# Kernel optimization log

Measured on AMD Instinct MI355X. Metric: run time of the kernel, lower is better.

Reference implementation:

```python
import jax, jax.numpy as jnp
import numpy as np

NUM_GRAPHS = 1024
IN_NODE = 128
OUT_GRAPH = 128
N_NODES = 500000

def _xavier(key, shape):
    fan_in, fan_out = shape[1], shape[0]
    a = float(np.sqrt(6.0 / (fan_in + fan_out)))
    return jax.random.uniform(key, shape, jnp.float32, -a, a)

def setup_inputs() -> dict:
    key = jax.random.key(0)
    k = jax.random.split(key, 5)
    x = jax.random.normal(k[0], (N_NODES, IN_NODE), jnp.float32)
    batch = jnp.sort(jax.random.randint(k[1], (N_NODES,), 0, NUM_GRAPHS))
    bias = jnp.full((OUT_GRAPH,), 0.01, jnp.float32)
    return {
        "x": x,
        "batch": batch,
        "W_lin": _xavier(k[2], (OUT_GRAPH, IN_NODE)),
        "b_lin": bias,
        "W_gate": _xavier(k[3], (OUT_GRAPH, IN_NODE)),
        "b_gate": bias,
        "W_final": _xavier(k[4], (OUT_GRAPH, OUT_GRAPH)),
        "b_final": bias,
    }

def reference(x, batch, W_lin, b_lin, W_gate, b_gate, W_final, b_final):
    # node projections: [N, out_graph]
    states = x @ W_lin.T + b_lin
    gates = jax.nn.softmax(x @ W_gate.T + b_gate, axis=1)  # softmax over feature dim
    gated = states * gates
    # scatter_mean over graph ids -> [num_graphs, out_graph]
    sums = jax.ops.segment_sum(gated, batch, num_segments=NUM_GRAPHS)
    counts = jax.ops.segment_sum(jnp.ones((gated.shape[0],), gated.dtype), batch, num_segments=NUM_GRAPHS)
    mean = sums / jnp.clip(counts, 1.0)[:, None]
    return mean @ W_final.T + b_final
```

## Files before the change

### kernel.cpp

```cpp
#include <hip/hip_runtime.h>

typedef __attribute__((ext_vector_type(8))) __bf16 bf16x8;
typedef __attribute__((ext_vector_type(4))) float f32x4;

__device__ __forceinline__ bf16x8 cvt8(f32x4 a, f32x4 b) {
    bf16x8 v;
    v[0] = (__bf16)a.x; v[1] = (__bf16)a.y; v[2] = (__bf16)a.z; v[3] = (__bf16)a.w;
    v[4] = (__bf16)b.x; v[5] = (__bf16)b.y; v[6] = (__bf16)b.z; v[7] = (__bf16)b.w;
    return v;
}

template <int CTRL>
__device__ __forceinline__ float dpp_addf(float v) {
    union { float f; int i; } s, r;
    s.f = v;
    r.i = __builtin_amdgcn_update_dpp(0, s.i, CTRL, 0xF, 0xF, true);
    return v + r.f;
}

__global__ void prep(const int* __restrict__ batch, int nN,
                     float* __restrict__ sums, int* __restrict__ off)
{
    const int i = blockIdx.x * blockDim.x + threadIdx.x;
    const int stride = gridDim.x * blockDim.x;
    for (int t = i; t < 1024 * 128; t += stride) sums[t] = 0.f;
    for (int t = i; t < nN; t += stride) {
        const int b  = batch[t];
        const int bp = (t == 0) ? -1 : batch[t - 1];
        for (int g = bp + 1; g <= b; ++g) off[g] = t;
        if (t == nN - 1) {
            for (int g = b + 1; g <= 1024; ++g) off[g] = nN;
        }
    }
}

__global__ __launch_bounds__(512, 2) void gnn_main(
    const float* __restrict__ x, const int* __restrict__ batch,
    const float* __restrict__ Wlin, const float* __restrict__ blin,
    const float* __restrict__ Wgate, const float* __restrict__ bgate,
    float* __restrict__ sums, int nN, int P)
{
    __shared__ __bf16 buf[2][32 * 128];
    __shared__ float  PS[8][36];
    __shared__ float  invLds[32];

    const int tid  = threadIdx.x;
    const int lane = tid & 63;
    const int w    = tid >> 6;
    const int l15  = lane & 15;
    const int lg   = lane >> 4;

    const int R0 = blockIdx.x * P;
    if (R0 >= nN) return;
    const int R1b = min(R0 + P, nN);
    const int nt  = (R1b - R0 + 31) >> 5;

    bf16x8 bfrag[2][4];
    {
        const float* Wp0 = Wlin  + (size_t)(w * 16 + l15) * 128 + lg * 8;
        const float* Wp1 = Wgate + (size_t)(w * 16 + l15) * 128 + lg * 8;
#pragma unroll
        for (int kk = 0; kk < 4; ++kk) {
            bfrag[0][kk] = cvt8(*(const f32x4*)(Wp0 + kk * 32),
                                *(const f32x4*)(Wp0 + kk * 32 + 4));
            bfrag[1][kk] = cvt8(*(const f32x4*)(Wp1 + kk * 32),
                                *(const f32x4*)(Wp1 + kk * 32 + 4));
        }
    }
    const float bl = blin[w * 16 + l15];
    const float bg = bgate[w * 16 + l15];

    const int srow = tid >> 4;
    const int skg  = tid & 15;
    f32x4 lv0, lv1;
    int   btn;
    auto stage_load = [&](int base) {
        const int nd = base + srow;
        const float* p = x + (size_t)(nd < nN ? nd : nN - 1) * 128 + skg * 8;
        lv0 = *(const f32x4*)p;
        lv1 = *(const f32x4*)(p + 4);
        const int bi = base + lane;
        btn = (bi < nN) ? batch[bi] : -1;
    };
    auto stage_write = [&](int bsel) {
        const int byte = (srow * 256 + skg * 16) ^ ((srow & 7) << 4);
        *(bf16x8*)((char*)&buf[bsel][0] + byte) = cvt8(lv0, lv1);
    };

    float racc = 0.f;
    int   gcur = batch[R0];
    auto flush = [&](int g) {
        float v = racc;
        v += __shfl_xor(v, 16);
        v += __shfl_xor(v, 32);
        if (lg == 0) atomicAdd(sums + (size_t)g * 128 + w * 16 + l15, v);
        racc = 0.f;
    };

    stage_load(R0);
    int bq0 = btn;
    stage_write(0);
    if (nt > 1) stage_load(R0 + 32);
    int bq1 = btn;
    asm volatile("s_waitcnt lgkmcnt(0)\n\ts_barrier" ::: "memory");

    for (int t = 0; t < nt; ++t) {
        const int base = R0 + (t << 5);

        f32x4 accS[2], accG[2];
#pragma unroll
        for (int r16 = 0; r16 < 2; ++r16) { accS[r16] = (f32x4)0.f; accG[r16] = (f32x4)0.f; }
        const char* bc = (const char*)&buf[t & 1][0];
#pragma unroll
        for (int kk = 0; kk < 4; ++kk) {
#pragma unroll
            for (int r16 = 0; r16 < 2; ++r16) {
                const int row  = r16 * 16 + l15;
                const int byte = (row * 256 + kk * 64 + lg * 16) ^ ((l15 & 7) << 4);
                bf16x8 af = *(const bf16x8*)(bc + byte);
                accS[r16] = __builtin_amdgcn_mfma_f32_16x16x32_bf16(af, bfrag[0][kk], accS[r16], 0, 0, 0);
                accG[r16] = __builtin_amdgcn_mfma_f32_16x16x32_bf16(af, bfrag[1][kk], accG[r16], 0, 0, 0);
            }
        }

#pragma unroll
        for (int r16 = 0; r16 < 2; ++r16) {
            f32x4 pv;
#pragma unroll
            for (int r = 0; r < 4; ++r) {
                float e = __expf(accG[r16][r] + bg);
                accG[r16][r] = e;
                float s = e;
                s = dpp_addf<0x128>(s);
                s = dpp_addf<0x124>(s);
                s = dpp_addf<0x122>(s);
                s = dpp_addf<0x121>(s);
                pv[r] = s;
            }
            if (l15 == 0) *(f32x4*)&PS[w][r16 * 16 + lg * 4] = pv;
        }

        if (t + 1 < nt) stage_write((t + 1) & 1);
        if (t + 2 < nt) stage_load(base + 64);
        asm volatile("s_waitcnt lgkmcnt(0)\n\ts_barrier" ::: "memory");

        {
            const int rw = w * 4 + (lane >> 4);
            float v = PS[lane & 7][rw];
            v = dpp_addf<0x124>(v);
            v = dpp_addf<0x4E>(v);
            v = dpp_addf<0xB1>(v);
            if ((lane & 15) == 0) invLds[rw] = 1.0f / v;
        }
        asm volatile("s_waitcnt lgkmcnt(0)\n\ts_barrier" ::: "memory");

#pragma unroll
        for (int r16 = 0; r16 < 2; ++r16) {
            f32x4 iv = *(const f32x4*)&invLds[r16 * 16 + lg * 4];
#pragma unroll
            for (int r = 0; r < 4; ++r)
                accS[r16][r] = (accS[r16][r] + bl) * accG[r16][r] * iv[r];
        }

        const int bt = bq0;
        const int nvalid = min(32, nN - base);
        const int gf = __builtin_amdgcn_readlane(bt, 0);
        const int gl = __builtin_amdgcn_readlane(bt, nvalid - 1);
        if (nvalid == 32 && gf == gl) {
            if (gf != gcur) { flush(gcur); gcur = gf; }
            float ts = 0.f;
#pragma unroll
            for (int r16 = 0; r16 < 2; ++r16)
#pragma unroll
                for (int r = 0; r < 4; ++r) ts += accS[r16][r];
            racc += ts;
        } else {
            for (int g = gf; g <= gl; ++g) {
                float cs = 0.f;
#pragma unroll
                for (int r16 = 0; r16 < 2; ++r16)
#pragma unroll
                    for (int r = 0; r < 4; ++r) {
                        const int bid = __shfl(bt, r16 * 16 + lg * 4 + r);
                        cs += (bid == g) ? accS[r16][r] : 0.f;
                    }
                if (g == gcur) racc += cs;
                else { flush(gcur); gcur = g; racc = cs; }
            }
        }
        bq0 = bq1;
        bq1 = btn;
    }
    flush(gcur);
}

__global__ __launch_bounds__(128) void final_mm(
    const float* __restrict__ sums, const int* __restrict__ off,
    const float* __restrict__ Wf, const float* __restrict__ bf,
    float* __restrict__ out)
{
    const int g = blockIdx.x, c = threadIdx.x;
    __shared__ float m[128];
    const int cnt = off[g + 1] - off[g];
    const float invC = 1.0f / (float)(cnt > 0 ? cnt : 1);
    m[c] = sums[g * 128 + c] * invC;
    __syncthreads();
    float acc = bf[c];
    const f32x4* wr = (const f32x4*)(Wf + (size_t)c * 128);
#pragma unroll
    for (int k = 0; k < 32; ++k) {
        f32x4 wv = wr[k];
        acc += m[4 * k] * wv.x + m[4 * k + 1] * wv.y + m[4 * k + 2] * wv.z + m[4 * k + 3] * wv.w;
    }
    out[g * 128 + c] = acc;
}

extern "C" void kernel_launch(void* const* d_in, const int* in_sizes, int n_in,
                              void* d_out, int out_size, void* d_ws, size_t ws_size,
                              hipStream_t stream)
{
    const float* x     = (const float*)d_in[0];
    const int*   batch = (const int*)d_in[1];
    const float* Wlin  = (const float*)d_in[2];
    const float* blin  = (const float*)d_in[3];
    const float* Wgate = (const float*)d_in[4];
    const float* bgate = (const float*)d_in[5];
    const float* Wfin  = (const float*)d_in[6];
    const float* bfin  = (const float*)d_in[7];
    float* out  = (float*)d_out;
    float* sums = (float*)d_ws;
    int*   off  = (int*)((char*)d_ws + 512 * 1024);

    const int nNodes  = in_sizes[1];
    const int nGraphs = out_size / 128;

    const int P  = ((((nNodes + 1023) / 1024) + 31) & ~31);
    const int nB = (nNodes + P - 1) / P;

    prep<<<1024, 256, 0, stream>>>(batch, nNodes, sums, off);
    gnn_main<<<nB, 512, 0, stream>>>(x, batch, Wlin, blin, Wgate, bgate, sums, nNodes, P);
    final_mm<<<nGraphs, 128, 0, stream>>>(sums, off, Wfin, bfin, out);
}
```

Before: 84.73 us.

## Use 256-thread blocks with 16-row tiles and 32 output columns per wave

Reshapes the main kernel from 8 waves over 32-row tiles to 4 waves over 16-row tiles, with each wave now covering 32 output features. Each A fragment loaded from LDS now feeds four MFMAs instead of two, and each block stages half as much data per step. The change also allows more blocks per CU and makes the per-row softmax reduction smaller. In exchange each wave holds twice as many weight fragments in registers, and the number of barriers per node roughly doubles because tiles are smaller.

Measured after the change: 98.42 us. 1.16x slower.

```diff
diff --git a/kernel.cpp b/kernel.cpp
--- a/kernel.cpp
+++ b/kernel.cpp
@@ -34,15 +34,15 @@
     }
 }
 
-__global__ __launch_bounds__(512, 2) void gnn_main(
+__global__ __launch_bounds__(256, 4) void gnn_main(
     const float* __restrict__ x, const int* __restrict__ batch,
     const float* __restrict__ Wlin, const float* __restrict__ blin,
     const float* __restrict__ Wgate, const float* __restrict__ bgate,
     float* __restrict__ sums, int nN, int P)
 {
-    __shared__ __bf16 buf[2][32 * 128];
-    __shared__ float  PS[8][36];
-    __shared__ float  invLds[32];
+    __shared__ __bf16 buf[2][16 * 128];
+    __shared__ float  PS[4][20];
+    __shared__ float  invLds[16];
 
     const int tid  = threadIdx.x;
     const int lane = tid & 63;
@@ -53,22 +53,27 @@
     const int R0 = blockIdx.x * P;
     if (R0 >= nN) return;
     const int R1b = min(R0 + P, nN);
-    const int nt  = (R1b - R0 + 31) >> 5;
-
-    bf16x8 bfrag[2][4];
-    {
-        const float* Wp0 = Wlin  + (size_t)(w * 16 + l15) * 128 + lg * 8;
-        const float* Wp1 = Wgate + (size_t)(w * 16 + l15) * 128 + lg * 8;
-#pragma unroll
-        for (int kk = 0; kk < 4; ++kk) {
-            bfrag[0][kk] = cvt8(*(const f32x4*)(Wp0 + kk * 32),
-                                *(const f32x4*)(Wp0 + kk * 32 + 4));
-            bfrag[1][kk] = cvt8(*(const f32x4*)(Wp1 + kk * 32),
-                                *(const f32x4*)(Wp1 + kk * 32 + 4));
-        }
-    }
-    const float bl = blin[w * 16 + l15];
-    const float bg = bgate[w * 16 + l15];
+    const int nt  = (R1b - R0 + 15) >> 4;
+
+    bf16x8 bfrag[2][2][4];
+#pragma unroll
+    for (int wt = 0; wt < 2; ++wt) {
+        const float* W = wt ? Wgate : Wlin;
+#pragma unroll
+        for (int ct = 0; ct < 2; ++ct) {
+            const float* Wp = W + (size_t)(w * 32 + ct * 16 + l15) * 128 + lg * 8;
+#pragma unroll
+            for (int kk = 0; kk < 4; ++kk)
+                bfrag[wt][ct][kk] = cvt8(*(const f32x4*)(Wp + kk * 32),
+                                         *(const f32x4*)(Wp + kk * 32 + 4));
+        }
+    }
+    float bl[2], bg[2];
+#pragma unroll
+    for (int ct = 0; ct < 2; ++ct) {
+        bl[ct] = blin[w * 32 + ct * 16 + l15];
+        bg[ct] = bgate[w * 32 + ct * 16 + l15];
+    }
 
     const int srow = tid >> 4;
     const int skg  = tid & 15;
@@ -79,7 +84,7 @@
         const float* p = x + (size_t)(nd < nN ? nd : nN - 1) * 128 + skg * 8;
         lv0 = *(const f32x4*)p;
         lv1 = *(const f32x4*)(p + 4);
-        const int bi = base + lane;
+        const int bi = base + l15;
         btn = (bi < nN) ? batch[bi] : -1;
     };
     auto stage_write = [&](int bsel) {
@@ -87,105 +92,104 @@
         *(bf16x8*)((char*)&buf[bsel][0] + byte) = cvt8(lv0, lv1);
     };
 
-    float racc = 0.f;
+    float racc[2] = {0.f, 0.f};
     int   gcur = batch[R0];
     auto flush = [&](int g) {
-        float v = racc;
-        v += __shfl_xor(v, 16);
-        v += __shfl_xor(v, 32);
-        if (lg == 0) atomicAdd(sums + (size_t)g * 128 + w * 16 + l15, v);
-        racc = 0.f;
+#pragma unroll
+        for (int ct = 0; ct < 2; ++ct) {
+            float v = racc[ct];
+            v += __shfl_xor(v, 16);
+            v += __shfl_xor(v, 32);
+            if (lg == 0) atomicAdd(sums + (size_t)g * 128 + w * 32 + ct * 16 + l15, v);
+            racc[ct] = 0.f;
+        }
     };
 
     stage_load(R0);
     int bq0 = btn;
     stage_write(0);
-    if (nt > 1) stage_load(R0 + 32);
+    if (nt > 1) stage_load(R0 + 16);
     int bq1 = btn;
     asm volatile("s_waitcnt lgkmcnt(0)\n\ts_barrier" ::: "memory");
 
     for (int t = 0; t < nt; ++t) {
-        const int base = R0 + (t << 5);
+        const int base = R0 + (t << 4);
 
         f32x4 accS[2], accG[2];
 #pragma unroll
-        for (int r16 = 0; r16 < 2; ++r16) { accS[r16] = (f32x4)0.f; accG[r16] = (f32x4)0.f; }
+        for (int ct = 0; ct < 2; ++ct) { accS[ct] = (f32x4)0.f; accG[ct] = (f32x4)0.f; }
         const char* bc = (const char*)&buf[t & 1][0];
 #pragma unroll
         for (int kk = 0; kk < 4; ++kk) {
-#pragma unroll
-            for (int r16 = 0; r16 < 2; ++r16) {
-                const int row  = r16 * 16 + l15;
-                const int byte = (row * 256 + kk * 64 + lg * 16) ^ ((l15 & 7) << 4);
-                bf16x8 af = *(const bf16x8*)(bc + byte);
-                accS[r16] = __builtin_amdgcn_mfma_f32_16x16x32_bf16(af, bfrag[0][kk], accS[r16], 0, 0, 0);
-                accG[r16] = __builtin_amdgcn_mfma_f32_16x16x32_bf16(af, bfrag[1][kk], accG[r16], 0, 0, 0);
+            const int byte = (l15 * 256 + kk * 64 + lg * 16) ^ ((l15 & 7) << 4);
+            bf16x8 af = *(const bf16x8*)(bc + byte);
+#pragma unroll
+            for (int ct = 0; ct < 2; ++ct) {
+                accS[ct] = __builtin_amdgcn_mfma_f32_16x16x32_bf16(af, bfrag[0][ct][kk], accS[ct], 0, 0, 0);
+                accG[ct] = __builtin_amdgcn_mfma_f32_16x16x32_bf16(af, bfrag[1][ct][kk], accG[ct], 0, 0, 0);
             }
         }
 
-#pragma unroll
-        for (int r16 = 0; r16 < 2; ++r16) {
+        {
             f32x4 pv;
 #pragma unroll
             for (int r = 0; r < 4; ++r) {
-                float e = __expf(accG[r16][r] + bg);
-                accG[r16][r] = e;
-                float s = e;
+                float e0 = __expf(accG[0][r] + bg[0]);
+                float e1 = __expf(accG[1][r] + bg[1]);
+                accG[0][r] = e0;
+                accG[1][r] = e1;
+                float s = e0 + e1;
                 s = dpp_addf<0x128>(s);
                 s = dpp_addf<0x124>(s);
                 s = dpp_addf<0x122>(s);
                 s = dpp_addf<0x121>(s);
                 pv[r] = s;
             }
-            if (l15 == 0) *(f32x4*)&PS[w][r16 * 16 + lg * 4] = pv;
+            if (l15 == 0) *(f32x4*)&PS[w][lg * 4] = pv;
         }
 
         if (t + 1 < nt) stage_write((t + 1) & 1);
-        if (t + 2 < nt) stage_load(base + 64);
+        if (t + 2 < nt) stage_load(base + 32);
         asm volatile("s_waitcnt lgkmcnt(0)\n\ts_barrier" ::: "memory");
 
         {
-            const int rw = w * 4 + (lane >> 4);
-            float v = PS[lane & 7][rw];
-            v = dpp_addf<0x124>(v);
+            float v = PS[lane & 3][lane >> 2];
+            v = dpp_addf<0xB1>(v);
             v = dpp_addf<0x4E>(v);
-            v = dpp_addf<0xB1>(v);
-            if ((lane & 15) == 0) invLds[rw] = 1.0f / v;
+            if ((lane & 3) == 0) invLds[lane >> 2] = 1.0f / v;
         }
         asm volatile("s_waitcnt lgkmcnt(0)\n\ts_barrier" ::: "memory");
 
-#pragma unroll
-        for (int r16 = 0; r16 < 2; ++r16) {
-            f32x4 iv = *(const f32x4*)&invLds[r16 * 16 + lg * 4];
-#pragma unroll
-            for (int r = 0; r < 4; ++r)
-                accS[r16][r] = (accS[r16][r] + bl) * accG[r16][r] * iv[r];
+        {
+            f32x4 iv = *(const f32x4*)&invLds[lg * 4];
+#pragma unroll
+            for (int ct = 0; ct < 2; ++ct)
+#pragma unroll
+                for (int r = 0; r < 4; ++r)
+                    accS[ct][r] = (accS[ct][r] + bl[ct]) * accG[ct][r] * iv[r];
         }
 
         const int bt = bq0;
-        const int nvalid = min(32, nN - base);
+        const int nvalid = min(16, nN - base);
         const int gf = __builtin_amdgcn_readlane(bt, 0);
         const int gl = __builtin_amdgcn_readlane(bt, nvalid - 1);
-        if (nvalid == 32 && gf == gl) {
+        if (nvalid == 16 && gf == gl) {
             if (gf != gcur) { flush(gcur); gcur = gf; }
-            float ts = 0.f;
-#pragma unroll
-            for (int r16 = 0; r16 < 2; ++r16)
-#pragma unroll
-                for (int r = 0; r < 4; ++r) ts += accS[r16][r];
-            racc += ts;
+#pragma unroll
+            for (int ct = 0; ct < 2; ++ct)
+                racc[ct] += (accS[ct][0] + accS[ct][1]) + (accS[ct][2] + accS[ct][3]);
         } else {
             for (int g = gf; g <= gl; ++g) {
-                float cs = 0.f;
-#pragma unroll
-                for (int r16 = 0; r16 < 2; ++r16)
-#pragma unroll
-                    for (int r = 0; r < 4; ++r) {
-                        const int bid = __shfl(bt, r16 * 16 + lg * 4 + r);
-                        cs += (bid == g) ? accS[r16][r] : 0.f;
-                    }
-                if (g == gcur) racc += cs;
-                else { flush(gcur); gcur = g; racc = cs; }
+                float cs0 = 0.f, cs1 = 0.f;
+#pragma unroll
+                for (int r = 0; r < 4; ++r) {
+                    const int bid = __shfl(bt, lg * 4 + r);
+                    cs0 += (bid == g) ? accS[0][r] : 0.f;
+                    cs1 += (bid == g) ? accS[1][r] : 0.f;
+                }
+                if (g != gcur) { flush(gcur); gcur = g; }
+                racc[0] += cs0;
+                racc[1] += cs1;
             }
         }
         bq0 = bq1;
@@ -234,10 +238,10 @@
     const int nNodes  = in_sizes[1];
     const int nGraphs = out_size / 128;
 
-    const int P  = ((((nNodes + 1023) / 1024) + 31) & ~31);
+    const int P  = ((((nNodes + 1023) / 1024) + 15) & ~15);
     const int nB = (nNodes + P - 1) / P;
 
     prep<<<1024, 256, 0, stream>>>(batch, nNodes, sums, off);
-    gnn_main<<<nB, 512, 0, stream>>>(x, batch, Wlin, blin, Wgate, bgate, sums, nNodes, P);
+    gnn_main<<<nB, 256, 0, stream>>>(x, batch, Wlin, blin, Wgate, bgate, sums, nNodes, P);
     final_mm<<<nGraphs, 128, 0, stream>>>(sums, off, Wfin, bfin, out);
 }
```

## Fuse per-graph counts into main kernel, drop prep kernel, batch final matmul

Applied to the files above, without the earlier changes.

Removes the prep kernel by computing per-graph node counts inside gnn_main with ballot/popcount and atomic adds. Zeroing of the workspace now uses hipMemsetAsync. The final matmul handles 8 graphs per block so each weight row is reused across them, and the launch bound asks for 4 blocks per SM. The aim is to cut one kernel launch and a pass over batch, at the cost of extra atomics and possible register pressure from the occupancy hint.

After: 85.73 us. About the same (+1.2%).

```diff
diff --git a/kernel.cpp b/kernel.cpp
--- a/kernel.cpp
+++ b/kernel.cpp
@@ -18,27 +18,11 @@
     return v + r.f;
 }
 
-__global__ void prep(const int* __restrict__ batch, int nN,
-                     float* __restrict__ sums, int* __restrict__ off)
-{
-    const int i = blockIdx.x * blockDim.x + threadIdx.x;
-    const int stride = gridDim.x * blockDim.x;
-    for (int t = i; t < 1024 * 128; t += stride) sums[t] = 0.f;
-    for (int t = i; t < nN; t += stride) {
-        const int b  = batch[t];
-        const int bp = (t == 0) ? -1 : batch[t - 1];
-        for (int g = bp + 1; g <= b; ++g) off[g] = t;
-        if (t == nN - 1) {
-            for (int g = b + 1; g <= 1024; ++g) off[g] = nN;
-        }
-    }
-}
-
-__global__ __launch_bounds__(512, 2) void gnn_main(
+__global__ __launch_bounds__(512, 4) void gnn_main(
     const float* __restrict__ x, const int* __restrict__ batch,
     const float* __restrict__ Wlin, const float* __restrict__ blin,
     const float* __restrict__ Wgate, const float* __restrict__ bgate,
-    float* __restrict__ sums, int nN, int P)
+    float* __restrict__ sums, float* __restrict__ counts, int nN, int P)
 {
     __shared__ __bf16 buf[2][32 * 128];
     __shared__ float  PS[8][36];
@@ -88,13 +72,16 @@
     };
 
     float racc = 0.f;
+    int   ncnt = 0;
     int   gcur = batch[R0];
     auto flush = [&](int g) {
         float v = racc;
         v += __shfl_xor(v, 16);
         v += __shfl_xor(v, 32);
         if (lg == 0) atomicAdd(sums + (size_t)g * 128 + w * 16 + l15, v);
+        if (w == 0 && lane == 0) atomicAdd(counts + g, (float)ncnt);
         racc = 0.f;
+        ncnt = 0;
     };
 
     stage_load(R0);
@@ -174,7 +161,10 @@
 #pragma unroll
                 for (int r = 0; r < 4; ++r) ts += accS[r16][r];
             racc += ts;
+            ncnt += 32;
         } else {
+            const unsigned long long vm =
+                (nvalid >= 64) ? ~0ull : ((1ull << nvalid) - 1ull);
             for (int g = gf; g <= gl; ++g) {
                 float cs = 0.f;
 #pragma unroll
@@ -184,8 +174,9 @@
                         const int bid = __shfl(bt, r16 * 16 + lg * 4 + r);
                         cs += (bid == g) ? accS[r16][r] : 0.f;
                     }
-                if (g == gcur) racc += cs;
-                else { flush(gcur); gcur = g; racc = cs; }
+                const int cg = __popcll(__ballot(bt == g) & vm);
+                if (g == gcur) { racc += cs; ncnt += cg; }
+                else { flush(gcur); gcur = g; racc = cs; ncnt = cg; }
             }
         }
         bq0 = bq1;
@@ -195,24 +186,35 @@
 }
 
 __global__ __launch_bounds__(128) void final_mm(
-    const float* __restrict__ sums, const int* __restrict__ off,
+    const float* __restrict__ sums, const float* __restrict__ counts,
     const float* __restrict__ Wf, const float* __restrict__ bf,
     float* __restrict__ out)
 {
-    const int g = blockIdx.x, c = threadIdx.x;
-    __shared__ float m[128];
-    const int cnt = off[g + 1] - off[g];
-    const float invC = 1.0f / (float)(cnt > 0 ? cnt : 1);
-    m[c] = sums[g * 128 + c] * invC;
+    const int c  = threadIdx.x;
+    const int g0 = blockIdx.x * 8;
+    __shared__ float m[8][128];
+#pragma unroll
+    for (int j = 0; j < 8; ++j) {
+        const float invC = 1.0f / fmaxf(counts[g0 + j], 1.0f);
+        m[j][c] = sums[(size_t)(g0 + j) * 128 + c] * invC;
+    }
     __syncthreads();
-    float acc = bf[c];
+    float acc[8];
+    const float b = bf[c];
+#pragma unroll
+    for (int j = 0; j < 8; ++j) acc[j] = b;
     const f32x4* wr = (const f32x4*)(Wf + (size_t)c * 128);
 #pragma unroll
     for (int k = 0; k < 32; ++k) {
         f32x4 wv = wr[k];
-        acc += m[4 * k] * wv.x + m[4 * k + 1] * wv.y + m[4 * k + 2] * wv.z + m[4 * k + 3] * wv.w;
-    }
-    out[g * 128 + c] = acc;
+#pragma unroll
+        for (int j = 0; j < 8; ++j) {
+            f32x4 mv = *(const f32x4*)&m[j][4 * k];
+            acc[j] += mv.x * wv.x + mv.y * wv.y + mv.z * wv.z + mv.w * wv.w;
+        }
+    }
+#pragma unroll
+    for (int j = 0; j < 8; ++j) out[(size_t)(g0 + j) * 128 + c] = acc[j];
 }
 
 extern "C" void kernel_launch(void* const* d_in, const int* in_sizes, int n_in,
@@ -227,9 +229,9 @@
     const float* bgate = (const float*)d_in[5];
     const float* Wfin  = (const float*)d_in[6];
     const float* bfin  = (const float*)d_in[7];
-    float* out  = (float*)d_out;
-    float* sums = (float*)d_ws;
-    int*   off  = (int*)((char*)d_ws + 512 * 1024);
+    float* out    = (float*)d_out;
+    float* sums   = (float*)d_ws;
+    float* counts = (float*)((char*)d_ws + 512 * 1024);
 
     const int nNodes  = in_sizes[1];
     const int nGraphs = out_size / 128;
@@ -237,7 +239,8 @@
     const int P  = ((((nNodes + 1023) / 1024) + 31) & ~31);
     const int nB = (nNodes + P - 1) / P;
 
-    prep<<<1024, 256, 0, stream>>>(batch, nNodes, sums, off);
-    gnn_main<<<nB, 512, 0, stream>>>(x, batch, Wlin, blin, Wgate, bgate, sums, nNodes, P);
-    final_mm<<<nGraphs, 128, 0, stream>>>(sums, off, Wfin, bfin, out);
-}
+    hipMemsetAsync(d_ws, 0, 512 * 1024 + 4096, stream);
+    gnn_main<<<nB, 512, 0, stream>>>(x, batch, Wlin, blin, Wgate, bgate,
+                                     sums, counts, nNodes, P);
+    final_mm<<<(nGraphs + 7) / 8, 128, 0, stream>>>(sums, counts, Wfin, bfin, out);
+}
```

## Software-pipeline softmax normalization and segment reduction one tile behind MFMA

Applied to the files above, without the earlier changes.

Each tile's un-normalized states and exp-gates are now parked in double-buffered LDS. The row-sum reciprocal and segment accumulation for tile t-1 run after the barrier of tile t, which removes one block barrier per tile and overlaps the epilogue with the next tile's MFMA and loads. The cost is much more LDS per block for the park buffers, extra LDS traffic, and exp values stored in bf16, which loses some precision.

Measured after the change: 91.94 us. +8.5%, slower.

```diff
diff --git a/kernel.cpp b/kernel.cpp
--- a/kernel.cpp
+++ b/kernel.cpp
@@ -41,8 +41,11 @@
     float* __restrict__ sums, int nN, int P)
 {
     __shared__ __bf16 buf[2][32 * 128];
-    __shared__ float  PS[8][36];
-    __shared__ float  invLds[32];
+    __shared__ float  parkS0[2][512 * 4];
+    __shared__ float  parkS1[2][512 * 4];
+    __shared__ __bf16 parkE[2][512 * 8];
+    __shared__ float  PS[2][8][36];
+    __shared__ float  invLds[2][32];
 
     const int tid  = threadIdx.x;
     const int lane = tid & 63;
@@ -97,20 +100,58 @@
         racc = 0.f;
     };
 
+    auto process = [&](int pt, int pb, int bt) {
+        bf16x8 Ev = *(const bf16x8*)&parkE[pb][tid * 8];
+        f32x4 s0 = *(const f32x4*)&parkS0[pb][tid * 4];
+        f32x4 s1 = *(const f32x4*)&parkS1[pb][tid * 4];
+        f32x4 iv0 = *(const f32x4*)&invLds[pb][lg * 4];
+        f32x4 iv1 = *(const f32x4*)&invLds[pb][16 + lg * 4];
+        f32x4 gs0, gs1;
+#pragma unroll
+        for (int r = 0; r < 4; ++r) {
+            gs0[r] = (s0[r] + bl) * (float)Ev[r]     * iv0[r];
+            gs1[r] = (s1[r] + bl) * (float)Ev[4 + r] * iv1[r];
+        }
+        const int base = R0 + (pt << 5);
+        const int nvalid = min(32, nN - base);
+        const int gf = __builtin_amdgcn_readlane(bt, 0);
+        const int gl = __builtin_amdgcn_readlane(bt, nvalid - 1);
+        if (nvalid == 32 && gf == gl) {
+            if (gf != gcur) { flush(gcur); gcur = gf; }
+            racc += (gs0[0] + gs0[1]) + (gs0[2] + gs0[3])
+                  + (gs1[0] + gs1[1]) + (gs1[2] + gs1[3]);
+        } else {
+            for (int g = gf; g <= gl; ++g) {
+                float cs = 0.f;
+#pragma unroll
+                for (int r = 0; r < 4; ++r) {
+                    const int b0 = __shfl(bt, lg * 4 + r);
+                    const int b1 = __shfl(bt, 16 + lg * 4 + r);
+                    cs += (b0 == g) ? gs0[r] : 0.f;
+                    cs += (b1 == g) ? gs1[r] : 0.f;
+                }
+                if (g == gcur) racc += cs;
+                else { flush(gcur); gcur = g; racc = cs; }
+            }
+        }
+    };
+
     stage_load(R0);
-    int bq0 = btn;
+    int bq_cur = btn;
     stage_write(0);
     if (nt > 1) stage_load(R0 + 32);
-    int bq1 = btn;
+    int bq_next = btn;
+    int bq_prev = 0;
     asm volatile("s_waitcnt lgkmcnt(0)\n\ts_barrier" ::: "memory");
 
     for (int t = 0; t < nt; ++t) {
+        const int cb = t & 1, pb = cb ^ 1;
         const int base = R0 + (t << 5);
 
         f32x4 accS[2], accG[2];
 #pragma unroll
         for (int r16 = 0; r16 < 2; ++r16) { accS[r16] = (f32x4)0.f; accG[r16] = (f32x4)0.f; }
-        const char* bc = (const char*)&buf[t & 1][0];
+        const char* bc = (const char*)&buf[cb][0];
 #pragma unroll
         for (int kk = 0; kk < 4; ++kk) {
 #pragma unroll
@@ -137,59 +178,44 @@
                 s = dpp_addf<0x121>(s);
                 pv[r] = s;
             }
-            if (l15 == 0) *(f32x4*)&PS[w][r16 * 16 + lg * 4] = pv;
-        }
-
-        if (t + 1 < nt) stage_write((t + 1) & 1);
-        if (t + 2 < nt) stage_load(base + 64);
-        asm volatile("s_waitcnt lgkmcnt(0)\n\ts_barrier" ::: "memory");
-
-        {
+            if (l15 == 0) *(f32x4*)&PS[cb][w][r16 * 16 + lg * 4] = pv;
+        }
+
+        *(bf16x8*)&parkE[cb][tid * 8] = cvt8(accG[0], accG[1]);
+        *(f32x4*)&parkS0[cb][tid * 4] = accS[0];
+        *(f32x4*)&parkS1[cb][tid * 4] = accS[1];
+
+        if (t > 0) {
             const int rw = w * 4 + (lane >> 4);
-            float v = PS[lane & 7][rw];
+            float v = PS[pb][lane & 7][rw];
             v = dpp_addf<0x124>(v);
             v = dpp_addf<0x4E>(v);
             v = dpp_addf<0xB1>(v);
-            if ((lane & 15) == 0) invLds[rw] = 1.0f / v;
-        }
+            if ((lane & 15) == 0) invLds[pb][rw] = 1.0f / v;
+        }
+
+        if (t + 1 < nt) stage_write((t + 1) & 1);
+        if (t + 2 < nt) stage_load(base + 64);
+
         asm volatile("s_waitcnt lgkmcnt(0)\n\ts_barrier" ::: "memory");
 
-#pragma unroll
-        for (int r16 = 0; r16 < 2; ++r16) {
-            f32x4 iv = *(const f32x4*)&invLds[r16 * 16 + lg * 4];
-#pragma unroll
-            for (int r = 0; r < 4; ++r)
-                accS[r16][r] = (accS[r16][r] + bl) * accG[r16][r] * iv[r];
-        }
-
-        const int bt = bq0;
-        const int nvalid = min(32, nN - base);
-        const int gf = __builtin_amdgcn_readlane(bt, 0);
-        const int gl = __builtin_amdgcn_readlane(bt, nvalid - 1);
-        if (nvalid == 32 && gf == gl) {
-            if (gf != gcur) { flush(gcur); gcur = gf; }
-            float ts = 0.f;
-#pragma unroll
-            for (int r16 = 0; r16 < 2; ++r16)
-#pragma unroll
-                for (int r = 0; r < 4; ++r) ts += accS[r16][r];
-            racc += ts;
-        } else {
-            for (int g = gf; g <= gl; ++g) {
-                float cs = 0.f;
-#pragma unroll
-                for (int r16 = 0; r16 < 2; ++r16)
-#pragma unroll
-                    for (int r = 0; r < 4; ++r) {
-                        const int bid = __shfl(bt, r16 * 16 + lg * 4 + r);
-                        cs += (bid == g) ? accS[r16][r] : 0.f;
-                    }
-                if (g == gcur) racc += cs;
-                else { flush(gcur); gcur = g; racc = cs; }
-            }
-        }
-        bq0 = bq1;
-        bq1 = btn;
+        if (t > 0) process(t - 1, pb, bq_prev);
+
+        bq_prev = bq_cur;
+        bq_cur  = bq_next;
+        bq_next = btn;
+    }
+
+    {
+        const int pb = (nt - 1) & 1;
+        const int rw = w * 4 + (lane >> 4);
+        float v = PS[pb][lane & 7][rw];
+        v = dpp_addf<0x124>(v);
+        v = dpp_addf<0x4E>(v);
+        v = dpp_addf<0xB1>(v);
+        if ((lane & 15) == 0) invLds[pb][rw] = 1.0f / v;
+        asm volatile("s_waitcnt lgkmcnt(0)\n\ts_barrier" ::: "memory");
+        process(nt - 1, pb, bq_prev);
     }
     flush(gcur);
 }
```
